# Kernel tuning notes

Measured on AMD Instinct MI355X. Metric: run time of the kernel, lower is better.

Reference implementation:

```python
import jax, jax.numpy as jnp
import numpy as np

EPS = 1e-5  # torch LayerNorm default

def ln(x, g, b):
    mu = jnp.mean(x, axis=-1, keepdims=True)
    var = jnp.mean((x - mu) ** 2, axis=-1, keepdims=True)
    return (x - mu) * jax.lax.rsqrt(var + EPS) * g + b

B, S, E, A = 131072, 199, 3, 32
D_IN = S + 1  # state_dim + 1 (time feature)

def setup_inputs() -> dict:
    key = jax.random.key(0)
    ks = iter(jax.random.split(key, 32))
    def w(shape, fan_in):
        lim = 1.0 / np.sqrt(fan_in)
        return jax.random.uniform(next(ks), shape, jnp.float32, -lim, lim)
    inp = {
        "state": jax.random.normal(next(ks), (B, S), jnp.float32),
        "time_delta": jax.random.uniform(next(ks), (B,), jnp.float32),
        # trunk: Linear(200,256)+LN, Linear(256,256)+LN, Linear(256,128)+LN
        "W1": w((D_IN, 256), D_IN), "b1": w((256,), D_IN),
        "g1": jnp.ones((256,), jnp.float32), "be1": jnp.zeros((256,), jnp.float32),
        "W2": w((256, 256), 256), "b2": w((256,), 256),
        "g2": jnp.ones((256,), jnp.float32), "be2": jnp.zeros((256,), jnp.float32),
        "W3": w((256, 128), 256), "b3": w((128,), 256),
        "g3": jnp.ones((128,), jnp.float32), "be3": jnp.zeros((128,), jnp.float32),
        # value stream
        "Wv1": w((128, 64), 128), "bv1": w((64,), 128),
        "gv": jnp.ones((64,), jnp.float32), "bev": jnp.zeros((64,), jnp.float32),
        "Wv2": w((64, 1), 64), "bv2": w((1,), 64),
        # E stacked advantage streams (all heads share action dim A)
        "Wa1": w((E, 128, 64), 128), "ba1": w((E, 64), 128),
        "ga": jnp.ones((E, 64), jnp.float32), "bea": jnp.zeros((E, 64), jnp.float32),
        "Wa2": w((E, 64, A), 64), "ba2": w((E, A), 64),
        "event_type": jax.random.randint(next(ks), (B,), 0, E),
    }
    return inp

def reference(state, time_delta,
              W1, b1, g1, be1, W2, b2, g2, be2, W3, b3, g3, be3,
              Wv1, bv1, gv, bev, Wv2, bv2,
              Wa1, ba1, ga, bea, Wa2, ba2, event_type):
    td = time_delta[:, None]                       # [B,1]
    x = jnp.concatenate([state, td], axis=1)       # [B,200]
    h = jax.nn.relu(ln(x @ W1 + b1, g1, be1))      # [B,256]
    h = jax.nn.relu(ln(h @ W2 + b2, g2, be2))      # [B,256]
    f = jax.nn.relu(ln(h @ W3 + b3, g3, be3))      # [B,128]
    v = jax.nn.relu(ln(f @ Wv1 + bv1, gv, bev)) @ Wv2 + bv2  # [B,1]
    # compute all E advantage heads, then per-sample select by event_type
    h1 = jnp.einsum('bd,edh->ebh', f, Wa1) + ba1[:, None, :]           # [E,B,64]
    h1 = jax.nn.relu(ln(h1, ga[:, None, :], bea[:, None, :]))
    adv_all = jnp.einsum('ebh,eha->eba', h1, Wa2) + ba2[:, None, :]    # [E,B,A]
    adv = jnp.take_along_axis(adv_all, event_type[None, :, None], axis=0)[0]  # [B,A]
    return v + (adv - adv.mean(axis=1, keepdims=True))
```

## Files before the change

### kernel.cpp

```cpp
#include <hip/hip_runtime.h>
#include <hip/hip_bf16.h>
#include <stdint.h>

#define DEV __device__ __forceinline__

typedef __attribute__((ext_vector_type(8))) short short8;
typedef __attribute__((ext_vector_type(4))) float floatx4;

constexpr int TM  = 64;
constexpr int NB  = 131072;
constexpr int AST = 264;

constexpr int OFF_W1 = 0;
constexpr int OFF_W2 = 57344;
constexpr int OFF_W3 = 122880;
constexpr int OFF_WH = 155648;
constexpr int OFF_WA2= 188416;
constexpr int NWQ    = 194560;

constexpr int C_B1=0, C_G1=256, C_BE1=512, C_B2=768, C_G2=1024, C_BE2=1280,
  C_B3=1536, C_G3=1664, C_BE3=1792, C_BV1=1920, C_GV=1984, C_BEV=2048,
  C_WV2=2112, C_BV2=2176, C_BA1=2177, C_GA=2369, C_BEA=2561, C_BA2=2753;
constexpr int NCONST=2849;

struct Ptrs {
  const float *state,*td,*W1,*b1,*g1,*be1,*W2,*b2,*g2,*be2,*W3,*b3,*g3,*be3,
    *Wv1,*bv1,*gv,*bev,*Wv2,*bv2,*Wa1,*ba1,*ga,*bea,*Wa2,*ba2;
  const int *et;
};

DEV unsigned short f2bf(float x){
  uint32_t u = __float_as_uint(x);
  u += 0x7fffu + ((u>>16)&1u);
  return (unsigned short)(u>>16);
}
DEV uint32_t f2bf_pk(float a, float b){
  float2 f2; f2.x=a; f2.y=b;
  __hip_bfloat162 h = __float22bfloat162_rn(f2);
  union { __hip_bfloat162 h; uint32_t u; } cv; cv.h = h;
  return cv.u;
}

__global__ void prep_kernel(Ptrs p, unsigned short* __restrict__ wq, float* __restrict__ cq){
  int idx = blockIdx.x*256 + threadIdx.x;
  if (idx < NWQ) {
    float v = 0.f;
    if (idx < OFF_W2) {
      int e = idx, w = e/14336, r = e%14336;
      int kc = r>>11, ct=(r>>9)&3, l=(r>>3)&63, j=r&7;
      int n = w*64 + ct*16 + (l&15);
      int k = kc*32 + (l>>4)*8 + j;
      if (k < 200) v = p.W1[k*256 + n];
      else if (k == 200) v = p.b1[n];
    } else if (idx < OFF_W3) {
      int e = idx-OFF_W2, w=e>>14, r=e&16383;
      int kc=r>>11, ct=(r>>9)&3, l=(r>>3)&63, j=r&7;
      int n = w*64 + ct*16 + (l&15);
      int k = kc*32 + (l>>4)*8 + j;
      int c = (k & ~63) + 16*(k&3) + ((k&63)>>2);
      v = p.W2[c*256 + n];
    } else if (idx < OFF_WH) {
      int e = idx-OFF_W3, w=e>>13, r=e&8191;
      int kc=r>>10, ct=(r>>9)&1, l=(r>>3)&63, j=r&7;
      int n = w*32 + ct*16 + (l&15);
      int k = kc*32 + (l>>4)*8 + j;
      int c = (k & ~63) + 16*(k&3) + ((k&63)>>2);
      v = p.W3[c*128 + n];
    } else if (idx < OFF_WA2) {
      int e = idx-OFF_WH, h=e>>13, r=e&8191;
      int kc=r>>11, ct=(r>>9)&3, l=(r>>3)&63, j=r&7;
      int n = ct*16 + (l&15);
      int k = kc*32 + (l>>4)*8 + j;
      int c = (k & ~31) + 16*(k&1) + ((k&31)>>1);
      v = (h<3) ? p.Wa1[h*8192 + c*64 + n] : p.Wv1[c*64 + n];
    } else {
      int e = idx-OFF_WA2, h=e>>11, r=e&2047;
      int kc=r>>10, ct=(r>>9)&1, l=(r>>3)&63, j=r&7;
      int n = ct*16 + (l&15);
      int k = kc*32 + (l>>4)*8 + j;
      int c = 16*(k&3) + (k>>2);
      v = p.Wa2[h*2048 + c*32 + n];
    }
    wq[idx] = f2bf(v);
  } else if (idx < NWQ + NCONST) {
    int ci = idx - NWQ;
    const float* src; int off;
    if      (ci < 256)  { src=p.b1;  off=ci; }
    else if (ci < 512)  { src=p.g1;  off=ci-256; }
    else if (ci < 768)  { src=p.be1; off=ci-512; }
    else if (ci < 1024) { src=p.b2;  off=ci-768; }
    else if (ci < 1280) { src=p.g2;  off=ci-1024; }
    else if (ci < 1536) { src=p.be2; off=ci-1280; }
    else if (ci < 1664) { src=p.b3;  off=ci-1536; }
    else if (ci < 1792) { src=p.g3;  off=ci-1664; }
    else if (ci < 1920) { src=p.be3; off=ci-1792; }
    else if (ci < 1984) { src=p.bv1; off=ci-1920; }
    else if (ci < 2048) { src=p.gv;  off=ci-1984; }
    else if (ci < 2112) { src=p.bev; off=ci-2048; }
    else if (ci < 2176) { src=p.Wv2; off=ci-2112; }
    else if (ci < 2177) { src=p.bv2; off=ci-2176; }
    else if (ci < 2369) { src=p.ba1; off=ci-2177; }
    else if (ci < 2561) { src=p.ga;  off=ci-2369; }
    else if (ci < 2753) { src=p.bea; off=ci-2561; }
    else                { src=p.ba2; off=ci-2753; }
    cq[ci] = src[off];
  }
}

template<int N>
DEV void loadB(short8 (&B)[N], const unsigned short* __restrict__ src, int lane){
  #pragma unroll
  for (int i=0;i<N;i++) B[i] = *(const short8*)(src + i*512 + lane*8);
}

template<int CT>
DEV void zeroAcc(floatx4 (&acc)[4][4]){
  const floatx4 z = {0.f,0.f,0.f,0.f};
  #pragma unroll
  for (int rt=0;rt<4;rt++)
    #pragma unroll
    for (int ct=0;ct<CT;ct++) acc[rt][ct]=z;
}

template<int KC,int CT>
DEV void runGemm(floatx4 (&acc)[4][4], const short8 (&B)[KC*CT],
                 const unsigned short* aBase, int aOff){
  #pragma unroll
  for (int kc=0;kc<KC;kc++){
    short8 a[4];
    #pragma unroll
    for (int rt=0;rt<4;rt++)
      a[rt] = *(const short8*)(aBase + rt*16*AST + aOff + kc*32);
    #pragma unroll
    for (int rt=0;rt<4;rt++)
      #pragma unroll
      for (int ct=0;ct<CT;ct++)
        acc[rt][ct] = __builtin_amdgcn_mfma_f32_16x16x32_bf16(a[rt], B[kc*CT+ct], acc[rt][ct], 0,0,0);
  }
}

template<int CT,bool BIAS>
DEV void statsAtomic(const floatx4 (&acc)[4][4], const float* __restrict__ cq, int bo, int colBase,
                     float* sbuf, float* ssbuf, int ln, int q, float (&bias)[4]){
  #pragma unroll
  for (int ct=0;ct<CT;ct++) bias[ct] = BIAS ? cq[bo+colBase+ct*16+ln] : 0.f;
  #pragma unroll
  for (int rt=0;rt<4;rt++){
    float s[4]={0,0,0,0}, ss[4]={0,0,0,0};
    #pragma unroll
    for (int ct=0;ct<CT;ct++){
      #pragma unroll
      for (int r=0;r<4;r++){
        float v=acc[rt][ct][r]+bias[ct];
        s[r]+=v; ss[r]+=v*v;
      }
    }
    #pragma unroll
    for (int r=0;r<4;r++){
      #pragma unroll
      for (int d=1;d<16;d<<=1){ s[r]+=__shfl_xor(s[r],d); ss[r]+=__shfl_xor(ss[r],d); }
      if (ln==0){
        int row = rt*16+q*4+r;
        atomicAdd(&sbuf[row],  s[r]);
        atomicAdd(&ssbuf[row], ss[r]);
      }
    }
  }
}

template<int CT>
DEV void lnWrite(const floatx4 (&acc)[4][4], const float* __restrict__ cq, int go, int beo, int colBase,
                 const float* sbuf, const float* ssbuf, float invN,
                 unsigned short* act_, int ln, int q, const float (&bias)[4]){
  float g[CT], be[CT];
  #pragma unroll
  for (int ct=0;ct<CT;ct++){ g[ct]=cq[go+colBase+ct*16+ln]; be[ct]=cq[beo+colBase+ct*16+ln]; }
  #pragma unroll
  for (int rt=0;rt<4;rt++){
    floatx4 sv  = *(const floatx4*)&sbuf [rt*16+q*4];
    floatx4 ssv = *(const floatx4*)&ssbuf[rt*16+q*4];
    #pragma unroll
    for (int r=0;r<4;r++){
      float mu = sv[r]*invN;
      float rs = rsqrtf(ssv[r]*invN - mu*mu + 1e-5f);
      int row=rt*16+q*4+r;
      unsigned short* pp = act_ + row*AST + colBase + ln*CT;
      float y[CT];
      #pragma unroll
      for (int ct=0;ct<CT;ct++)
        y[ct] = fmaxf((acc[rt][ct][r]+bias[ct]-mu)*rs*g[ct]+be[ct], 0.f);
      if constexpr (CT==4){
        uint2 pk; pk.x = f2bf_pk(y[0],y[1]); pk.y = f2bf_pk(y[2],y[3]);
        *(uint2*)pp = pk;
      } else {
        *(uint32_t*)pp = f2bf_pk(y[0],y[1]);
      }
    }
  }
}

__global__ __launch_bounds__(256,4) void dqn_main(
    const float* __restrict__ state, const float* __restrict__ td,
    const int* __restrict__ et, const unsigned short* __restrict__ wq,
    const float* __restrict__ cq, float* __restrict__ out)
{
  __shared__ __align__(16) unsigned short act[TM*AST];
  __shared__ float sstat[2][2][64];
  __shared__ float vbuf[64];
  __shared__ int   etl[64];

  const int tid=threadIdx.x, w=tid>>6, lane=tid&63, q=lane>>4, ln=lane&15;
  const int rowBlk = blockIdx.x*TM;

  {
    ((float*)sstat)[tid] = 0.f;
    const float* sbase = state + (size_t)rowBlk*199;
    for (int i=tid; i<64*199; i+=256){
      float v = sbase[i];
      int row = i/199, col = i - row*199;
      act[row*AST+col] = f2bf(v);
    }
    for (int i=tid; i<64*32; i+=256){
      int row = i>>5, c = 199 + (i&31);
      unsigned short hv = 0;
      if (c==199) hv = f2bf(td[rowBlk+row]);
      else if (c==200) hv = 0x3F80u;
      act[row*AST+c] = hv;
    }
    if (tid < 64) etl[tid] = et[rowBlk+tid];
  }
  __syncthreads();

  const unsigned short* aBase = act + ln*AST + q*8;
  floatx4 acc[4][4];
  float bias[4];

  {
    short8 B[28];
    loadB<28>(B, wq + OFF_W1 + w*14336, lane);
    zeroAcc<4>(acc);
    runGemm<7,4>(acc, B, aBase, 0);
  }
  statsAtomic<4,false>(acc, cq, 0, w*64, sstat[0][0], sstat[0][1], ln, q, bias);
  __syncthreads();
  lnWrite<4>(acc, cq, C_G1, C_BE1, w*64, sstat[0][0], sstat[0][1], 1.f/256.f, act, ln, q, bias);
  __syncthreads();

  {
    short8 B[32];
    loadB<32>(B, wq + OFF_W2 + w*16384, lane);
    zeroAcc<4>(acc);
    runGemm<8,4>(acc, B, aBase, 0);
  }
  statsAtomic<4,true>(acc, cq, C_B2, w*64, sstat[1][0], sstat[1][1], ln, q, bias);
  __syncthreads();
  if (tid < 128) ((float*)sstat[0])[tid] = 0.f;
  lnWrite<4>(acc, cq, C_G2, C_BE2, w*64, sstat[1][0], sstat[1][1], 1.f/256.f, act, ln, q, bias);
  __syncthreads();

  {
    short8 B[16];
    loadB<16>(B, wq + OFF_W3 + w*8192, lane);
    zeroAcc<2>(acc);
    runGemm<8,2>(acc, B, aBase, 0);
  }
  statsAtomic<2,true>(acc, cq, C_B3, w*32, sstat[0][0], sstat[0][1], ln, q, bias);
  __syncthreads();
  lnWrite<2>(acc, cq, C_G3, C_BE3, w*32, sstat[0][0], sstat[0][1], 1.f/128.f, act, ln, q, bias);
  __syncthreads();

  {
    short8 B[16];
    loadB<16>(B, wq + OFF_WH + w*8192, lane);
    zeroAcc<4>(acc);
    runGemm<4,4>(acc, B, aBase, 0);
  }
  {
    const int bo = (w<3)? C_BA1+w*64 : C_BV1;
    const int go = (w<3)? C_GA +w*64 : C_GV;
    const int beo= (w<3)? C_BEA+w*64 : C_BEV;
    float bi[4], g[4], be[4];
    #pragma unroll
    for (int ct=0;ct<4;ct++){ bi[ct]=cq[bo+ct*16+ln]; g[ct]=cq[go+ct*16+ln]; be[ct]=cq[beo+ct*16+ln]; }
    float wv[4]; float bv2v = 0.f;
    if (w==3){
      #pragma unroll
      for (int ct=0;ct<4;ct++) wv[ct]=cq[C_WV2+ct*16+ln];
      bv2v = cq[C_BV2];
    }
    #pragma unroll
    for (int rt=0;rt<4;rt++){
      float y[4][4];
      float s[4]={0,0,0,0}, ss[4]={0,0,0,0};
      #pragma unroll
      for (int ct=0;ct<4;ct++)
        #pragma unroll
        for (int r=0;r<4;r++){
          float v=acc[rt][ct][r]+bi[ct];
          y[ct][r]=v; s[r]+=v; ss[r]+=v*v;
        }
      #pragma unroll
      for (int r=0;r<4;r++){
        #pragma unroll
        for (int d=1;d<16;d<<=1){ s[r]+=__shfl_xor(s[r],d); ss[r]+=__shfl_xor(ss[r],d); }
        float mu=s[r]*(1.f/64.f);
        float rs=rsqrtf(ss[r]*(1.f/64.f)-mu*mu+1e-5f);
        #pragma unroll
        for (int ct=0;ct<4;ct++)
          y[ct][r]=fmaxf((y[ct][r]-mu)*rs*g[ct]+be[ct], 0.f);
      }

      if (w==3){
        float dd[4]={0,0,0,0};
        #pragma unroll
        for (int ct=0;ct<4;ct++)
          #pragma unroll
          for (int r=0;r<4;r++) dd[r]+=y[ct][r]*wv[ct];
        #pragma unroll
        for (int r=0;r<4;r++){
          #pragma unroll
          for (int d=1;d<16;d<<=1) dd[r]+=__shfl_xor(dd[r],d);
          if (ln==0) vbuf[rt*16+q*4+r]=dd[r]+bv2v;
        }
      } else {
        #pragma unroll
        for (int r=0;r<4;r++){
          int row=rt*16+q*4+r;
          (void)row;
        }
      }
      if (w<3){
        #pragma unroll
        for (int ct=0;ct<4;ct++)
          #pragma unroll
          for (int r=0;r<4;r++) acc[rt][ct][r]=y[ct][r];
      }
    }
  }
  __syncthreads();

  if (w<3){
    #pragma unroll
    for (int rt=0;rt<4;rt++)
      #pragma unroll
      for (int r=0;r<4;r++){
        int row=rt*16+q*4+r;
        unsigned short* pp = act + row*AST + 64*w + ln*4;
        uint2 pk;
        pk.x = f2bf_pk(acc[rt][0][r], acc[rt][1][r]);
        pk.y = f2bf_pk(acc[rt][2][r], acc[rt][3][r]);
        *(uint2*)pp = pk;
      }
    short8 B2[4];
    loadB<4>(B2, wq + OFF_WA2 + w*2048, lane);
    zeroAcc<2>(acc);
    runGemm<2,2>(acc, B2, aBase, 64*w);
    float b20 = cq[C_BA2 + w*32 + ln];
    float b21 = cq[C_BA2 + w*32 + 16 + ln];
    #pragma unroll
    for (int rt=0;rt<4;rt++)
      #pragma unroll
      for (int r=0;r<4;r++){
        float a0 = acc[rt][0][r] + b20;
        float a1 = acc[rt][1][r] + b21;
        float sm = a0 + a1;
        #pragma unroll
        for (int d=1;d<16;d<<=1) sm += __shfl_xor(sm,d);
        int row = rt*16+q*4+r;
        if (etl[row]==w){
          float vv = vbuf[row];
          float m  = sm*(1.f/32.f);
          float* op = out + (size_t)(rowBlk+row)*32 + ln;
          op[0]  = vv + a0 - m;
          op[16] = vv + a1 - m;
        }
      }
  }
}

extern "C" void kernel_launch(void* const* d_in, const int* in_sizes, int n_in,
                              void* d_out, int out_size, void* d_ws, size_t ws_size,
                              hipStream_t stream)
{
  Ptrs p;
  p.state=(const float*)d_in[0];  p.td =(const float*)d_in[1];
  p.W1 =(const float*)d_in[2];  p.b1 =(const float*)d_in[3];  p.g1 =(const float*)d_in[4];  p.be1=(const float*)d_in[5];
  p.W2 =(const float*)d_in[6];  p.b2 =(const float*)d_in[7];  p.g2 =(const float*)d_in[8];  p.be2=(const float*)d_in[9];
  p.W3 =(const float*)d_in[10]; p.b3 =(const float*)d_in[11]; p.g3 =(const float*)d_in[12]; p.be3=(const float*)d_in[13];
  p.Wv1=(const float*)d_in[14]; p.bv1=(const float*)d_in[15]; p.gv =(const float*)d_in[16]; p.bev=(const float*)d_in[17];
  p.Wv2=(const float*)d_in[18]; p.bv2=(const float*)d_in[19];
  p.Wa1=(const float*)d_in[20]; p.ba1=(const float*)d_in[21]; p.ga =(const float*)d_in[22]; p.bea=(const float*)d_in[23];
  p.Wa2=(const float*)d_in[24]; p.ba2=(const float*)d_in[25];
  p.et =(const int*)d_in[26];

  unsigned short* wq = (unsigned short*)d_ws;
  float* cq = (float*)((char*)d_ws + (size_t)NWQ*2);

  const int prepN = NWQ + NCONST;
  hipLaunchKernelGGL(prep_kernel, dim3((prepN+255)/256), dim3(256), 0, stream, p, wq, cq);
  hipLaunchKernelGGL(dqn_main, dim3(NB/TM), dim3(256), 0, stream,
                     p.state, p.td, p.et, (const unsigned short*)wq, (const float*)cq, (float*)d_out);
}
```

Measured before the change: 309.2 us.

## Transpose MFMA operand roles so features land in rows and samples in columns

```diff
diff --git a/kernel.cpp b/kernel.cpp
--- a/kernel.cpp
+++ b/kernel.cpp
@@ -20,8 +20,8 @@
 
 constexpr int C_B1=0, C_G1=256, C_BE1=512, C_B2=768, C_G2=1024, C_BE2=1280,
   C_B3=1536, C_G3=1664, C_BE3=1792, C_BV1=1920, C_GV=1984, C_BEV=2048,
-  C_WV2=2112, C_BV2=2176, C_BA1=2177, C_GA=2369, C_BEA=2561, C_BA2=2753;
-constexpr int NCONST=2849;
+  C_WV2=2112, C_BV2=2176, C_BA1=2180, C_GA=2372, C_BEA=2564, C_BA2=2756;
+constexpr int NCONST=2852;
 
 struct Ptrs {
   const float *state,*td,*W1,*b1,*g1,*be1,*W2,*b2,*g2,*be2,*W3,*b3,*g3,*be3,
@@ -57,53 +57,49 @@
       int kc=r>>11, ct=(r>>9)&3, l=(r>>3)&63, j=r&7;
       int n = w*64 + ct*16 + (l&15);
       int k = kc*32 + (l>>4)*8 + j;
-      int c = (k & ~63) + 16*(k&3) + ((k&63)>>2);
-      v = p.W2[c*256 + n];
+      v = p.W2[k*256 + n];
     } else if (idx < OFF_WH) {
       int e = idx-OFF_W3, w=e>>13, r=e&8191;
       int kc=r>>10, ct=(r>>9)&1, l=(r>>3)&63, j=r&7;
       int n = w*32 + ct*16 + (l&15);
       int k = kc*32 + (l>>4)*8 + j;
-      int c = (k & ~63) + 16*(k&3) + ((k&63)>>2);
-      v = p.W3[c*128 + n];
+      v = p.W3[k*128 + n];
     } else if (idx < OFF_WA2) {
       int e = idx-OFF_WH, h=e>>13, r=e&8191;
       int kc=r>>11, ct=(r>>9)&3, l=(r>>3)&63, j=r&7;
       int n = ct*16 + (l&15);
       int k = kc*32 + (l>>4)*8 + j;
-      int c = (k & ~31) + 16*(k&1) + ((k&31)>>1);
-      v = (h<3) ? p.Wa1[h*8192 + c*64 + n] : p.Wv1[c*64 + n];
+      v = (h<3) ? p.Wa1[h*8192 + k*64 + n] : p.Wv1[k*64 + n];
     } else {
       int e = idx-OFF_WA2, h=e>>11, r=e&2047;
       int kc=r>>10, ct=(r>>9)&1, l=(r>>3)&63, j=r&7;
       int n = ct*16 + (l&15);
       int k = kc*32 + (l>>4)*8 + j;
-      int c = 16*(k&3) + (k>>2);
-      v = p.Wa2[h*2048 + c*32 + n];
+      v = p.Wa2[h*2048 + k*32 + n];
     }
     wq[idx] = f2bf(v);
   } else if (idx < NWQ + NCONST) {
     int ci = idx - NWQ;
-    const float* src; int off;
-    if      (ci < 256)  { src=p.b1;  off=ci; }
-    else if (ci < 512)  { src=p.g1;  off=ci-256; }
-    else if (ci < 768)  { src=p.be1; off=ci-512; }
-    else if (ci < 1024) { src=p.b2;  off=ci-768; }
-    else if (ci < 1280) { src=p.g2;  off=ci-1024; }
-    else if (ci < 1536) { src=p.be2; off=ci-1280; }
-    else if (ci < 1664) { src=p.b3;  off=ci-1536; }
-    else if (ci < 1792) { src=p.g3;  off=ci-1664; }
-    else if (ci < 1920) { src=p.be3; off=ci-1792; }
-    else if (ci < 1984) { src=p.bv1; off=ci-1920; }
-    else if (ci < 2048) { src=p.gv;  off=ci-1984; }
-    else if (ci < 2112) { src=p.bev; off=ci-2048; }
-    else if (ci < 2176) { src=p.Wv2; off=ci-2112; }
-    else if (ci < 2177) { src=p.bv2; off=ci-2176; }
-    else if (ci < 2369) { src=p.ba1; off=ci-2177; }
-    else if (ci < 2561) { src=p.ga;  off=ci-2369; }
-    else if (ci < 2753) { src=p.bea; off=ci-2561; }
-    else                { src=p.ba2; off=ci-2753; }
-    cq[ci] = src[off];
+    float v;
+    if      (ci < 256)  v = p.b1[ci];
+    else if (ci < 512)  v = p.g1[ci-256];
+    else if (ci < 768)  v = p.be1[ci-512];
+    else if (ci < 1024) v = p.b2[ci-768];
+    else if (ci < 1280) v = p.g2[ci-1024];
+    else if (ci < 1536) v = p.be2[ci-1280];
+    else if (ci < 1664) v = p.b3[ci-1536];
+    else if (ci < 1792) v = p.g3[ci-1664];
+    else if (ci < 1920) v = p.be3[ci-1792];
+    else if (ci < 1984) v = p.bv1[ci-1920];
+    else if (ci < 2048) v = p.gv[ci-1984];
+    else if (ci < 2112) v = p.bev[ci-2048];
+    else if (ci < 2176) v = p.Wv2[ci-2112];
+    else if (ci < 2180) v = (ci==2176) ? p.bv2[0] : 0.f;
+    else if (ci < 2372) v = p.ba1[ci-2180];
+    else if (ci < 2564) v = p.ga[ci-2372];
+    else if (ci < 2756) v = p.bea[ci-2564];
+    else                v = p.ba2[ci-2756];
+    cq[ci] = v;
   }
 }
 
@@ -113,88 +109,82 @@
   for (int i=0;i<N;i++) B[i] = *(const short8*)(src + i*512 + lane*8);
 }
 
-template<int CT>
-DEV void zeroAcc(floatx4 (&acc)[4][4]){
+template<int RT>
+DEV void zeroAccT(floatx4 (&acc)[RT][4]){
   const floatx4 z = {0.f,0.f,0.f,0.f};
   #pragma unroll
-  for (int rt=0;rt<4;rt++)
-    #pragma unroll
-    for (int ct=0;ct<CT;ct++) acc[rt][ct]=z;
-}
-
-template<int KC,int CT>
-DEV void runGemm(floatx4 (&acc)[4][4], const short8 (&B)[KC*CT],
-                 const unsigned short* aBase, int aOff){
+  for (int rt=0;rt<RT;rt++)
+    #pragma unroll
+    for (int ct=0;ct<4;ct++) acc[rt][ct]=z;
+}
+
+template<int KC,int RT>
+DEV void runGemmT(floatx4 (&acc)[RT][4], const short8 (&Bw)[KC*RT],
+                  const unsigned short* aBase, int aOff){
   #pragma unroll
   for (int kc=0;kc<KC;kc++){
     short8 a[4];
     #pragma unroll
-    for (int rt=0;rt<4;rt++)
-      a[rt] = *(const short8*)(aBase + rt*16*AST + aOff + kc*32);
-    #pragma unroll
-    for (int rt=0;rt<4;rt++)
-      #pragma unroll
-      for (int ct=0;ct<CT;ct++)
-        acc[rt][ct] = __builtin_amdgcn_mfma_f32_16x16x32_bf16(a[rt], B[kc*CT+ct], acc[rt][ct], 0,0,0);
-  }
-}
-
-template<int CT,bool BIAS>
-DEV void statsAtomic(const floatx4 (&acc)[4][4], const float* __restrict__ cq, int bo, int colBase,
-                     float* sbuf, float* ssbuf, int ln, int q, float (&bias)[4]){
-  #pragma unroll
-  for (int ct=0;ct<CT;ct++) bias[ct] = BIAS ? cq[bo+colBase+ct*16+ln] : 0.f;
-  #pragma unroll
-  for (int rt=0;rt<4;rt++){
-    float s[4]={0,0,0,0}, ss[4]={0,0,0,0};
-    #pragma unroll
-    for (int ct=0;ct<CT;ct++){
-      #pragma unroll
-      for (int r=0;r<4;r++){
-        float v=acc[rt][ct][r]+bias[ct];
-        s[r]+=v; ss[r]+=v*v;
-      }
-    }
-    #pragma unroll
-    for (int r=0;r<4;r++){
-      #pragma unroll
-      for (int d=1;d<16;d<<=1){ s[r]+=__shfl_xor(s[r],d); ss[r]+=__shfl_xor(ss[r],d); }
-      if (ln==0){
-        int row = rt*16+q*4+r;
-        atomicAdd(&sbuf[row],  s[r]);
-        atomicAdd(&ssbuf[row], ss[r]);
-      }
-    }
-  }
-}
-
-template<int CT>
-DEV void lnWrite(const floatx4 (&acc)[4][4], const float* __restrict__ cq, int go, int beo, int colBase,
-                 const float* sbuf, const float* ssbuf, float invN,
-                 unsigned short* act_, int ln, int q, const float (&bias)[4]){
-  float g[CT], be[CT];
-  #pragma unroll
-  for (int ct=0;ct<CT;ct++){ g[ct]=cq[go+colBase+ct*16+ln]; be[ct]=cq[beo+colBase+ct*16+ln]; }
-  #pragma unroll
-  for (int rt=0;rt<4;rt++){
-    floatx4 sv  = *(const floatx4*)&sbuf [rt*16+q*4];
-    floatx4 ssv = *(const floatx4*)&ssbuf[rt*16+q*4];
-    #pragma unroll
-    for (int r=0;r<4;r++){
-      float mu = sv[r]*invN;
-      float rs = rsqrtf(ssv[r]*invN - mu*mu + 1e-5f);
-      int row=rt*16+q*4+r;
-      unsigned short* pp = act_ + row*AST + colBase + ln*CT;
-      float y[CT];
-      #pragma unroll
-      for (int ct=0;ct<CT;ct++)
-        y[ct] = fmaxf((acc[rt][ct][r]+bias[ct]-mu)*rs*g[ct]+be[ct], 0.f);
-      if constexpr (CT==4){
-        uint2 pk; pk.x = f2bf_pk(y[0],y[1]); pk.y = f2bf_pk(y[2],y[3]);
-        *(uint2*)pp = pk;
-      } else {
-        *(uint32_t*)pp = f2bf_pk(y[0],y[1]);
-      }
+    for (int ct=0;ct<4;ct++)
+      a[ct] = *(const short8*)(aBase + ct*16*AST + aOff + kc*32);
+    #pragma unroll
+    for (int rt=0;rt<RT;rt++)
+      #pragma unroll
+      for (int ct=0;ct<4;ct++)
+        acc[rt][ct] = __builtin_amdgcn_mfma_f32_16x16x32_bf16(Bw[kc*RT+rt], a[ct], acc[rt][ct], 0,0,0);
+  }
+}
+
+template<int RT,bool BIAS>
+DEV void statsT(floatx4 (&acc)[RT][4], const float* __restrict__ cq, int bo,
+                float* sbuf, float* ssbuf, int q, int ln){
+  if constexpr (BIAS){
+    #pragma unroll
+    for (int rt=0;rt<RT;rt++){
+      floatx4 b4 = *(const floatx4*)(cq + bo + rt*16 + q*4);
+      #pragma unroll
+      for (int ct=0;ct<4;ct++) acc[rt][ct] += b4;
+    }
+  }
+  #pragma unroll
+  for (int ct=0;ct<4;ct++){
+    float s=0.f, ss=0.f;
+    #pragma unroll
+    for (int rt=0;rt<RT;rt++)
+      #pragma unroll
+      for (int r=0;r<4;r++){ float v=acc[rt][ct][r]; s+=v; ss+=v*v; }
+    s += __shfl_xor(s,16); ss += __shfl_xor(ss,16);
+    s += __shfl_xor(s,32); ss += __shfl_xor(ss,32);
+    if (q==0){
+      atomicAdd(&sbuf[ct*16+ln], s);
+      atomicAdd(&ssbuf[ct*16+ln], ss);
+    }
+  }
+}
+
+template<int RT>
+DEV void lnWriteT(const floatx4 (&acc)[RT][4], const float* __restrict__ cq, int go, int beo,
+                  const float* sbuf, const float* ssbuf, float invN,
+                  unsigned short* act_, int colBase, int q, int ln){
+  float mu[4], rs[4];
+  #pragma unroll
+  for (int ct=0;ct<4;ct++){
+    float sv = sbuf[ct*16+ln], ssv = ssbuf[ct*16+ln];
+    mu[ct] = sv*invN;
+    rs[ct] = rsqrtf(ssv*invN - mu[ct]*mu[ct] + 1e-5f);
+  }
+  #pragma unroll
+  for (int rt=0;rt<RT;rt++){
+    floatx4 g4  = *(const floatx4*)(cq + go  + rt*16 + q*4);
+    floatx4 be4 = *(const floatx4*)(cq + beo + rt*16 + q*4);
+    #pragma unroll
+    for (int ct=0;ct<4;ct++){
+      float y[4];
+      #pragma unroll
+      for (int r=0;r<4;r++)
+        y[r] = fmaxf((acc[rt][ct][r]-mu[ct])*rs[ct]*g4[r]+be4[r], 0.f);
+      uint2 pk; pk.x = f2bf_pk(y[0],y[1]); pk.y = f2bf_pk(y[2],y[3]);
+      *(uint2*)(act_ + (ct*16+ln)*AST + colBase + rt*16 + q*4) = pk;
     }
   }
 }
@@ -215,17 +205,27 @@
   {
     ((float*)sstat)[tid] = 0.f;
     const float* sbase = state + (size_t)rowBlk*199;
-    for (int i=tid; i<64*199; i+=256){
-      float v = sbase[i];
-      int row = i/199, col = i - row*199;
-      act[row*AST+col] = f2bf(v);
-    }
-    for (int i=tid; i<64*32; i+=256){
-      int row = i>>5, c = 199 + (i&31);
-      unsigned short hv = 0;
-      if (c==199) hv = f2bf(td[rowBlk+row]);
-      else if (c==200) hv = 0x3F80u;
-      act[row*AST+c] = hv;
+    #pragma unroll
+    for (int it=0; it<7; ++it){
+      int t = tid + it*256;
+      int r = t/28, c = t - r*28;
+      unsigned short* dst = act + r*AST + c*8;
+      if (c < 25){
+        const float* src = sbase + r*199 + c*8;
+        float v0=src[0], v1=src[1], v2=src[2], v3=src[3];
+        float v4=src[4], v5=src[5], v6=src[6];
+        int o7 = (c==24)? 198 : c*8+7;
+        float s7 = sbase[r*199 + o7];
+        float v7 = (c==24)? td[rowBlk+r] : s7;
+        uint4 pk;
+        pk.x=f2bf_pk(v0,v1); pk.y=f2bf_pk(v2,v3);
+        pk.z=f2bf_pk(v4,v5); pk.w=f2bf_pk(v6,v7);
+        *(uint4*)dst = pk;
+      } else {
+        uint4 pk{0u,0u,0u,0u};
+        if (c==25) pk.x = 0x3F80u;
+        *(uint4*)dst = pk;
+      }
     }
     if (tid < 64) etl[tid] = et[rowBlk+tid];
   }
@@ -233,108 +233,97 @@
 
   const unsigned short* aBase = act + ln*AST + q*8;
   floatx4 acc[4][4];
-  float bias[4];
-
-  {
-    short8 B[28];
-    loadB<28>(B, wq + OFF_W1 + w*14336, lane);
-    zeroAcc<4>(acc);
-    runGemm<7,4>(acc, B, aBase, 0);
-  }
-  statsAtomic<4,false>(acc, cq, 0, w*64, sstat[0][0], sstat[0][1], ln, q, bias);
-  __syncthreads();
-  lnWrite<4>(acc, cq, C_G1, C_BE1, w*64, sstat[0][0], sstat[0][1], 1.f/256.f, act, ln, q, bias);
-  __syncthreads();
-
-  {
-    short8 B[32];
-    loadB<32>(B, wq + OFF_W2 + w*16384, lane);
-    zeroAcc<4>(acc);
-    runGemm<8,4>(acc, B, aBase, 0);
-  }
-  statsAtomic<4,true>(acc, cq, C_B2, w*64, sstat[1][0], sstat[1][1], ln, q, bias);
+
+  {
+    short8 Bw[28];
+    loadB<28>(Bw, wq + OFF_W1 + w*14336, lane);
+    zeroAccT<4>(acc);
+    runGemmT<7,4>(acc, Bw, aBase, 0);
+  }
+  statsT<4,false>(acc, cq, 0, sstat[0][0], sstat[0][1], q, ln);
+  __syncthreads();
+  lnWriteT<4>(acc, cq, C_G1+w*64, C_BE1+w*64, sstat[0][0], sstat[0][1], 1.f/256.f, act, w*64, q, ln);
+  __syncthreads();
+
+  {
+    short8 Bw[32];
+    loadB<32>(Bw, wq + OFF_W2 + w*16384, lane);
+    zeroAccT<4>(acc);
+    runGemmT<8,4>(acc, Bw, aBase, 0);
+  }
+  statsT<4,true>(acc, cq, C_B2+w*64, sstat[1][0], sstat[1][1], q, ln);
   __syncthreads();
   if (tid < 128) ((float*)sstat[0])[tid] = 0.f;
-  lnWrite<4>(acc, cq, C_G2, C_BE2, w*64, sstat[1][0], sstat[1][1], 1.f/256.f, act, ln, q, bias);
-  __syncthreads();
-
-  {
-    short8 B[16];
-    loadB<16>(B, wq + OFF_W3 + w*8192, lane);
-    zeroAcc<2>(acc);
-    runGemm<8,2>(acc, B, aBase, 0);
-  }
-  statsAtomic<2,true>(acc, cq, C_B3, w*32, sstat[0][0], sstat[0][1], ln, q, bias);
-  __syncthreads();
-  lnWrite<2>(acc, cq, C_G3, C_BE3, w*32, sstat[0][0], sstat[0][1], 1.f/128.f, act, ln, q, bias);
-  __syncthreads();
-
-  {
-    short8 B[16];
-    loadB<16>(B, wq + OFF_WH + w*8192, lane);
-    zeroAcc<4>(acc);
-    runGemm<4,4>(acc, B, aBase, 0);
+  lnWriteT<4>(acc, cq, C_G2+w*64, C_BE2+w*64, sstat[1][0], sstat[1][1], 1.f/256.f, act, w*64, q, ln);
+  __syncthreads();
+
+  floatx4 acc3[2][4];
+  {
+    short8 Bw[16];
+    loadB<16>(Bw, wq + OFF_W3 + w*8192, lane);
+    zeroAccT<2>(acc3);
+    runGemmT<8,2>(acc3, Bw, aBase, 0);
+  }
+  statsT<2,true>(acc3, cq, C_B3+w*32, sstat[0][0], sstat[0][1], q, ln);
+  __syncthreads();
+  lnWriteT<2>(acc3, cq, C_G3+w*32, C_BE3+w*32, sstat[0][0], sstat[0][1], 1.f/128.f, act, w*32, q, ln);
+  __syncthreads();
+
+  {
+    short8 Bh[16];
+    loadB<16>(Bh, wq + OFF_WH + w*8192, lane);
+    zeroAccT<4>(acc);
+    runGemmT<4,4>(acc, Bh, aBase, 0);
   }
   {
     const int bo = (w<3)? C_BA1+w*64 : C_BV1;
     const int go = (w<3)? C_GA +w*64 : C_GV;
     const int beo= (w<3)? C_BEA+w*64 : C_BEV;
-    float bi[4], g[4], be[4];
-    #pragma unroll
-    for (int ct=0;ct<4;ct++){ bi[ct]=cq[bo+ct*16+ln]; g[ct]=cq[go+ct*16+ln]; be[ct]=cq[beo+ct*16+ln]; }
-    float wv[4]; float bv2v = 0.f;
+    #pragma unroll
+    for (int rt=0;rt<4;rt++){
+      floatx4 b4 = *(const floatx4*)(cq + bo + rt*16 + q*4);
+      #pragma unroll
+      for (int ct=0;ct<4;ct++) acc[rt][ct] += b4;
+    }
+    float mu[4], rs[4];
+    #pragma unroll
+    for (int ct=0;ct<4;ct++){
+      float s=0.f, ss=0.f;
+      #pragma unroll
+      for (int rt=0;rt<4;rt++)
+        #pragma unroll
+        for (int r=0;r<4;r++){ float v=acc[rt][ct][r]; s+=v; ss+=v*v; }
+      s += __shfl_xor(s,16); ss += __shfl_xor(ss,16);
+      s += __shfl_xor(s,32); ss += __shfl_xor(ss,32);
+      mu[ct]=s*(1.f/64.f);
+      rs[ct]=rsqrtf(ss*(1.f/64.f)-mu[ct]*mu[ct]+1e-5f);
+    }
+    #pragma unroll
+    for (int rt=0;rt<4;rt++){
+      floatx4 g4  = *(const floatx4*)(cq + go  + rt*16 + q*4);
+      floatx4 be4 = *(const floatx4*)(cq + beo + rt*16 + q*4);
+      #pragma unroll
+      for (int ct=0;ct<4;ct++)
+        #pragma unroll
+        for (int r=0;r<4;r++)
+          acc[rt][ct][r] = fmaxf((acc[rt][ct][r]-mu[ct])*rs[ct]*g4[r]+be4[r], 0.f);
+    }
     if (w==3){
-      #pragma unroll
-      for (int ct=0;ct<4;ct++) wv[ct]=cq[C_WV2+ct*16+ln];
-      bv2v = cq[C_BV2];
-    }
-    #pragma unroll
-    for (int rt=0;rt<4;rt++){
-      float y[4][4];
-      float s[4]={0,0,0,0}, ss[4]={0,0,0,0};
-      #pragma unroll
-      for (int ct=0;ct<4;ct++)
-        #pragma unroll
-        for (int r=0;r<4;r++){
-          float v=acc[rt][ct][r]+bi[ct];
-          y[ct][r]=v; s[r]+=v; ss[r]+=v*v;
-        }
-      #pragma unroll
-      for (int r=0;r<4;r++){
-        #pragma unroll
-        for (int d=1;d<16;d<<=1){ s[r]+=__shfl_xor(s[r],d); ss[r]+=__shfl_xor(ss[r],d); }
-        float mu=s[r]*(1.f/64.f);
-        float rs=rsqrtf(ss[r]*(1.f/64.f)-mu*mu+1e-5f);
-        #pragma unroll
-        for (int ct=0;ct<4;ct++)
-          y[ct][r]=fmaxf((y[ct][r]-mu)*rs*g[ct]+be[ct], 0.f);
+      float bv2v = cq[C_BV2];
+      floatx4 wv4[4];
+      #pragma unroll
+      for (int rt=0;rt<4;rt++) wv4[rt] = *(const floatx4*)(cq + C_WV2 + rt*16 + q*4);
+      #pragma unroll
+      for (int ct=0;ct<4;ct++){
+        float dot=0.f;
+        #pragma unroll
+        for (int rt=0;rt<4;rt++)
+          #pragma unroll
+          for (int r=0;r<4;r++) dot += acc[rt][ct][r]*wv4[rt][r];
+        dot += __shfl_xor(dot,16);
+        dot += __shfl_xor(dot,32);
+        if (q==0) vbuf[ct*16+ln] = dot + bv2v;
       }
-
-      if (w==3){
-        float dd[4]={0,0,0,0};
-        #pragma unroll
-        for (int ct=0;ct<4;ct++)
-          #pragma unroll
-          for (int r=0;r<4;r++) dd[r]+=y[ct][r]*wv[ct];
-        #pragma unroll
-        for (int r=0;r<4;r++){
-          #pragma unroll
-          for (int d=1;d<16;d<<=1) dd[r]+=__shfl_xor(dd[r],d);
-          if (ln==0) vbuf[rt*16+q*4+r]=dd[r]+bv2v;
-        }
-      } else {
-        #pragma unroll
-        for (int r=0;r<4;r++){
-          int row=rt*16+q*4+r;
-          (void)row;
-        }
-      }
-      if (w<3){
-        #pragma unroll
-        for (int ct=0;ct<4;ct++)
-          #pragma unroll
-          for (int r=0;r<4;r++) acc[rt][ct][r]=y[ct][r];
-      }
     }
   }
   __syncthreads();
@@ -343,38 +332,43 @@
     #pragma unroll
     for (int rt=0;rt<4;rt++)
       #pragma unroll
-      for (int r=0;r<4;r++){
-        int row=rt*16+q*4+r;
-        unsigned short* pp = act + row*AST + 64*w + ln*4;
+      for (int ct=0;ct<4;ct++){
         uint2 pk;
-        pk.x = f2bf_pk(acc[rt][0][r], acc[rt][1][r]);
-        pk.y = f2bf_pk(acc[rt][2][r], acc[rt][3][r]);
-        *(uint2*)pp = pk;
+        pk.x = f2bf_pk(acc[rt][ct][0], acc[rt][ct][1]);
+        pk.y = f2bf_pk(acc[rt][ct][2], acc[rt][ct][3]);
+        *(uint2*)(act + (ct*16+ln)*AST + 64*w + rt*16 + q*4) = pk;
       }
     short8 B2[4];
     loadB<4>(B2, wq + OFF_WA2 + w*2048, lane);
-    zeroAcc<2>(acc);
-    runGemm<2,2>(acc, B2, aBase, 64*w);
-    float b20 = cq[C_BA2 + w*32 + ln];
-    float b21 = cq[C_BA2 + w*32 + 16 + ln];
-    #pragma unroll
-    for (int rt=0;rt<4;rt++)
-      #pragma unroll
-      for (int r=0;r<4;r++){
-        float a0 = acc[rt][0][r] + b20;
-        float a1 = acc[rt][1][r] + b21;
-        float sm = a0 + a1;
-        #pragma unroll
-        for (int d=1;d<16;d<<=1) sm += __shfl_xor(sm,d);
-        int row = rt*16+q*4+r;
-        if (etl[row]==w){
-          float vv = vbuf[row];
-          float m  = sm*(1.f/32.f);
-          float* op = out + (size_t)(rowBlk+row)*32 + ln;
-          op[0]  = vv + a0 - m;
-          op[16] = vv + a1 - m;
+    floatx4 acc2[2][4];
+    zeroAccT<2>(acc2);
+    runGemmT<2,2>(acc2, B2, aBase, 64*w);
+    #pragma unroll
+    for (int rt=0;rt<2;rt++){
+      floatx4 b4 = *(const floatx4*)(cq + C_BA2 + w*32 + rt*16 + q*4);
+      #pragma unroll
+      for (int ct=0;ct<4;ct++) acc2[rt][ct] += b4;
+    }
+    #pragma unroll
+    for (int ct=0;ct<4;ct++){
+      float sm=0.f;
+      #pragma unroll
+      for (int rt=0;rt<2;rt++)
+        #pragma unroll
+        for (int r=0;r<4;r++) sm += acc2[rt][ct][r];
+      sm += __shfl_xor(sm,16);
+      sm += __shfl_xor(sm,32);
+      int b = ct*16+ln;
+      if (etl[b]==w){
+        float vm = vbuf[b] - sm*(1.f/32.f);
+        #pragma unroll
+        for (int rt=0;rt<2;rt++){
+          floatx4 o = acc2[rt][ct];
+          o[0]+=vm; o[1]+=vm; o[2]+=vm; o[3]+=vm;
+          *(floatx4*)(out + (size_t)(rowBlk+b)*32 + rt*16 + q*4) = o;
         }
       }
+    }
   }
 }
 
```

New measurement: 284.8 us. 1.09x faster.
